# Kernel optimization log

Measured on AMD Instinct MI355X. Metric: run time of the kernel, lower is better.

Reference implementation:

```python
import jax, jax.numpy as jnp
import numpy as np

N, E, L, D = 4, 64, 512, 256


def setup_inputs() -> dict:
    key = jax.random.key(0)
    k1, k2, k3 = jax.random.split(key, 3)
    doc_state = jax.random.normal(k1, (N, L, D), dtype=jnp.float32)
    nodes_mapping = (jax.random.uniform(k2, (N, E, L)) < 0.1).astype(jnp.float32)
    # entity lengths = number of selected tokens (some may be 0, exercising the guard)
    nodes_len = jnp.sum(nodes_mapping, axis=2)  # N x E, float32
    return {"doc_state": doc_state, "nodes_mapping": nodes_mapping, "nodes_len": nodes_len}


def reference(doc_state, nodes_mapping, nodes_len):
    # entity_states: N x E x L x d = mask-broadcast of token states
    entity_states = nodes_mapping[:, :, :, None] * doc_state[:, None, :, :]
    max_pooled = jnp.max(entity_states, axis=2)          # N x E x d
    safe_len = jnp.where(nodes_len > 0, nodes_len, jnp.ones_like(nodes_len))
    mean_pooled = jnp.sum(entity_states, axis=2) / safe_len[:, :, None]  # N x E x d
    return jnp.concatenate([max_pooled, mean_pooled], axis=2)  # N x E x 2d
```

## Files before the change

### kernel.cpp

```cpp
#include <hip/hip_runtime.h>
#include <math.h>

#define PN 4
#define PE 64
#define PL 512
#define PD 256
#define NWAVES 16
#define TOK_PER_WAVE (PL / NWAVES)

__global__ __launch_bounds__(64 * NWAVES) void MeanMaxPooling_84473416778475_kernel(
    const float* __restrict__ doc_state,
    const float* __restrict__ nodes_mapping,
    const float* __restrict__ nodes_len,
    float* __restrict__ out)
{
    const int ne   = blockIdx.x;
    const int n    = ne >> 6;
    const int e    = ne & 63;
    const int tid  = threadIdx.x;
    const int w    = tid >> 6;
    const int lane = tid & 63;

    __shared__ float  smask[PL];
    __shared__ float4 s_sum[NWAVES][64];
    __shared__ float4 s_max[NWAVES][64];

    if (tid < PL) {
        smask[tid] = nodes_mapping[(size_t)(n * PE + e) * PL + tid];
    }
    __syncthreads();

    const float4* ds = (const float4*)(doc_state + (size_t)n * PL * PD);

    float4 sum = make_float4(0.f, 0.f, 0.f, 0.f);
    float4 mx  = make_float4(-INFINITY, -INFINITY, -INFINITY, -INFINITY);

    const int l0 = w * TOK_PER_WAVE;
    #pragma unroll 8
    for (int i = 0; i < TOK_PER_WAVE; ++i) {
        const int l = l0 + i;
        const float  m = smask[l];
        const float4 s = ds[l * 64 + lane];
        const float vx = m * s.x, vy = m * s.y, vz = m * s.z, vw = m * s.w;
        sum.x += vx; sum.y += vy; sum.z += vz; sum.w += vw;
        mx.x = fmaxf(mx.x, vx);
        mx.y = fmaxf(mx.y, vy);
        mx.z = fmaxf(mx.z, vz);
        mx.w = fmaxf(mx.w, vw);
    }

    s_sum[w][lane] = sum;
    s_max[w][lane] = mx;
    __syncthreads();

    if (tid < 64) {
        float4 tsum = s_sum[0][lane];
        float4 tmax = s_max[0][lane];
        #pragma unroll
        for (int j = 1; j < NWAVES; ++j) {
            const float4 s2 = s_sum[j][lane];
            const float4 m2 = s_max[j][lane];
            tsum.x += s2.x; tsum.y += s2.y; tsum.z += s2.z; tsum.w += s2.w;
            tmax.x = fmaxf(tmax.x, m2.x);
            tmax.y = fmaxf(tmax.y, m2.y);
            tmax.z = fmaxf(tmax.z, m2.z);
            tmax.w = fmaxf(tmax.w, m2.w);
        }
        const float len  = nodes_len[n * PE + e];
        const float slen = (len > 0.f) ? len : 1.0f;
        float4 mean;
        mean.x = tsum.x / slen;
        mean.y = tsum.y / slen;
        mean.z = tsum.z / slen;
        mean.w = tsum.w / slen;

        float4* o = (float4*)(out + (size_t)(n * PE + e) * 2 * PD);
        o[lane]      = tmax;
        o[64 + lane] = mean;
    }
}

extern "C" void kernel_launch(void* const* d_in, const int* in_sizes, int n_in,
                              void* d_out, int out_size, void* d_ws, size_t ws_size,
                              hipStream_t stream) {
    const float* doc_state     = (const float*)d_in[0];
    const float* nodes_mapping = (const float*)d_in[1];
    const float* nodes_len     = (const float*)d_in[2];
    float* out = (float*)d_out;

    dim3 grid(PN * PE);
    dim3 block(64 * NWAVES);
    MeanMaxPooling_84473416778475_kernel<<<grid, block, 0, stream>>>(
        doc_state, nodes_mapping, nodes_len, out);
}
```

Before: 63.43 us.

## Compact selected tokens into an index list and only gather those rows

```diff
diff --git a/kernel.cpp b/kernel.cpp
--- a/kernel.cpp
+++ b/kernel.cpp
@@ -5,10 +5,10 @@
 #define PE 64
 #define PL 512
 #define PD 256
-#define NWAVES 16
-#define TOK_PER_WAVE (PL / NWAVES)
+#define NW 16
+#define NTHREADS (64 * NW)
 
-__global__ __launch_bounds__(64 * NWAVES) void MeanMaxPooling_84473416778475_kernel(
+__global__ __launch_bounds__(NTHREADS) void MeanMaxPooling_84473416778475_kernel(
     const float* __restrict__ doc_state,
     const float* __restrict__ nodes_mapping,
     const float* __restrict__ nodes_len,
@@ -21,32 +21,64 @@
     const int w    = tid >> 6;
     const int lane = tid & 63;
 
-    __shared__ float  smask[PL];
-    __shared__ float4 s_sum[NWAVES][64];
-    __shared__ float4 s_max[NWAVES][64];
+    __shared__ int    sidx[PL];
+    __shared__ int    wcnt[NW];
+    __shared__ int    woff[NW];
+    __shared__ int    stotal;
+    __shared__ float4 s_sum[NW][64];
+    __shared__ float4 s_max[NW][64];
 
+    bool sel = false;
     if (tid < PL) {
-        smask[tid] = nodes_mapping[(size_t)(n * PE + e) * PL + tid];
+        const float m = nodes_mapping[(size_t)(n * PE + e) * PL + tid];
+        sel = (m > 0.5f);
+    }
+    const unsigned long long b = __ballot(sel);
+    if (lane == 0) wcnt[w] = (int)__popcll(b);
+    __syncthreads();
+    if (tid == 0) {
+        int acc = 0;
+        #pragma unroll
+        for (int j = 0; j < NW; ++j) { woff[j] = acc; acc += wcnt[j]; }
+        stotal = acc;
+    }
+    __syncthreads();
+    if (sel) {
+        const int pos = woff[w] + (int)__popcll(b & ((1ull << lane) - 1ull));
+        sidx[pos] = tid;
     }
     __syncthreads();
 
-    const float4* ds = (const float4*)(doc_state + (size_t)n * PL * PD);
+    const int total = stotal;
+
+    const float4* __restrict__ ds = (const float4*)(doc_state + (size_t)n * PL * PD);
 
     float4 sum = make_float4(0.f, 0.f, 0.f, 0.f);
     float4 mx  = make_float4(-INFINITY, -INFINITY, -INFINITY, -INFINITY);
 
-    const int l0 = w * TOK_PER_WAVE;
-    #pragma unroll 8
-    for (int i = 0; i < TOK_PER_WAVE; ++i) {
-        const int l = l0 + i;
-        const float  m = smask[l];
-        const float4 s = ds[l * 64 + lane];
-        const float vx = m * s.x, vy = m * s.y, vz = m * s.z, vw = m * s.w;
-        sum.x += vx; sum.y += vy; sum.z += vz; sum.w += vw;
-        mx.x = fmaxf(mx.x, vx);
-        mx.y = fmaxf(mx.y, vy);
-        mx.z = fmaxf(mx.z, vz);
-        mx.w = fmaxf(mx.w, vw);
+    auto acc1 = [&](const float4 s) {
+        sum.x += s.x; sum.y += s.y; sum.z += s.z; sum.w += s.w;
+        mx.x = fmaxf(mx.x, s.x);
+        mx.y = fmaxf(mx.y, s.y);
+        mx.z = fmaxf(mx.z, s.z);
+        mx.w = fmaxf(mx.w, s.w);
+    };
+
+    int i = w;
+    for (; i + 3 * NW < total; i += 4 * NW) {
+        const int l0 = sidx[i];
+        const int l1 = sidx[i + NW];
+        const int l2 = sidx[i + 2 * NW];
+        const int l3 = sidx[i + 3 * NW];
+        const float4 s0 = ds[l0 * 64 + lane];
+        const float4 s1 = ds[l1 * 64 + lane];
+        const float4 s2 = ds[l2 * 64 + lane];
+        const float4 s3 = ds[l3 * 64 + lane];
+        acc1(s0); acc1(s1); acc1(s2); acc1(s3);
+    }
+    for (; i < total; i += NW) {
+        const float4 s = ds[sidx[i] * 64 + lane];
+        acc1(s);
     }
 
     s_sum[w][lane] = sum;
@@ -57,7 +89,7 @@
         float4 tsum = s_sum[0][lane];
         float4 tmax = s_max[0][lane];
         #pragma unroll
-        for (int j = 1; j < NWAVES; ++j) {
+        for (int j = 1; j < NW; ++j) {
             const float4 s2 = s_sum[j][lane];
             const float4 m2 = s_max[j][lane];
             tsum.x += s2.x; tsum.y += s2.y; tsum.z += s2.z; tsum.w += s2.w;
@@ -65,6 +97,12 @@
             tmax.y = fmaxf(tmax.y, m2.y);
             tmax.z = fmaxf(tmax.z, m2.z);
             tmax.w = fmaxf(tmax.w, m2.w);
+        }
+        if (total < PL) {
+            tmax.x = fmaxf(tmax.x, 0.f);
+            tmax.y = fmaxf(tmax.y, 0.f);
+            tmax.z = fmaxf(tmax.z, 0.f);
+            tmax.w = fmaxf(tmax.w, 0.f);
         }
         const float len  = nodes_len[n * PE + e];
         const float slen = (len > 0.f) ? len : 1.0f;
@@ -89,7 +127,7 @@
     float* out = (float*)d_out;
 
     dim3 grid(PN * PE);
-    dim3 block(64 * NWAVES);
+    dim3 block(NTHREADS);
     MeanMaxPooling_84473416778475_kernel<<<grid, block, 0, stream>>>(
         doc_state, nodes_mapping, nodes_len, out);
 }
```

Measured after the change: 59.46 us. 1.07x faster.
